# Kernel tuning notes

Hardware: AMD Instinct MI355X
Metric: run time of the kernel (lower is better)

The kernel has to match this reference:

```python
import jax, jax.numpy as jnp
import numpy as np

B, T, D = 8, 1024, 768
H, DH = 12, 64
E, K, DFF = 16, 2, 3072
EPS = 1e-5


def _ln(x, w, b):
    m = x.mean(-1, keepdims=True)
    v = ((x - m) ** 2).mean(-1, keepdims=True)
    return (x - m) * jax.lax.rsqrt(v + EPS) * w + b


def setup_inputs() -> dict:
    key = jax.random.key(0)
    ks = jax.random.split(key, 12)
    s = 0.02
    return {
        "x": jax.random.normal(ks[0], (B, T, D), jnp.float32),
        "ln1_w": jnp.ones((D,), jnp.float32),
        "ln1_b": jnp.zeros((D,), jnp.float32),
        "qkv_w": jax.random.normal(ks[1], (D, 3 * D), jnp.float32) * s,
        "qkv_b": jnp.zeros((3 * D,), jnp.float32),
        "proj_w": jax.random.normal(ks[2], (D, D), jnp.float32) * s,
        "proj_b": jnp.zeros((D,), jnp.float32),
        "ln2_w": jnp.ones((D,), jnp.float32),
        "ln2_b": jnp.zeros((D,), jnp.float32),
        "router_w": jax.random.normal(ks[3], (D, E), jnp.float32) * s,
        "w1": jax.random.normal(ks[4], (E, D, DFF), jnp.float32) * s,
        "b1": jnp.zeros((E, DFF), jnp.float32),
        "w2": jax.random.normal(ks[5], (E, DFF, D), jnp.float32) * s,
        "b2": jnp.zeros((E, D), jnp.float32),
    }


def _block(x, ln1_w, ln1_b, qkv_w, qkv_b, proj_w, proj_b,
           ln2_w, ln2_b, router_w, w1, b1, w2, b2):
    # --- attention ---
    h = _ln(x, ln1_w, ln1_b)
    qkv = h @ qkv_w + qkv_b                      # [B,T,3D]
    q, k, v = jnp.split(qkv, 3, axis=-1)
    q = q.reshape(B, T, H, DH).transpose(0, 2, 1, 3)
    k = k.reshape(B, T, H, DH).transpose(0, 2, 1, 3)
    v = v.reshape(B, T, H, DH).transpose(0, 2, 1, 3)
    scores = jnp.einsum("bhqd,bhkd->bhqk", q, k) / np.sqrt(DH)
    causal = jnp.tril(jnp.ones((T, T), bool))
    scores = jnp.where(causal, scores, -jnp.inf)
    attn = jax.nn.softmax(scores, axis=-1)
    y = jnp.einsum("bhqk,bhkd->bhqd", attn, v)
    y = y.transpose(0, 2, 1, 3).reshape(B, T, D)
    x = x + y @ proj_w + proj_b                  # residual 1

    # --- MoE FFN (dense all-experts, gated combine) ---
    z = _ln(x, ln2_w, ln2_b)                     # [B,T,D]
    probs = jax.nn.softmax(z @ router_w, axis=-1)  # [B,T,E]
    top_p, ix = jax.lax.top_k(probs, K)
    gate = (jax.nn.one_hot(ix, E, dtype=probs.dtype) * top_p[..., None]).sum(-2)  # [B,T,E]
    gate_e = jnp.moveaxis(gate, -1, 0)           # [E,B,T]

    def body(acc, ew):
        g, W1, B1, W2, B2 = ew
        out = jax.nn.gelu(z @ W1 + B1, approximate=False) @ W2 + B2
        return acc + g[..., None] * out, None

    yff, _ = jax.lax.scan(body, jnp.zeros_like(z), (gate_e, w1, b1, w2, b2))
    # MoELayer returns z + yff; Block adds x again (faithful double residual)
    return x + z + yff


def reference(x, ln1_w, ln1_b, qkv_w, qkv_b, proj_w, proj_b,
              ln2_w, ln2_b, router_w, w1, b1, w2, b2):
    return _block(x, ln1_w, ln1_b, qkv_w, qkv_b, proj_w, proj_b,
                  ln2_w, ln2_b, router_w, w1, b1, w2, b2)
```

## Files before the change

### kernel.cpp

```cpp
#include <hip/hip_runtime.h>
#include <math.h>

#define D_MODEL 768
#define T_SEQ   1024
#define B_BATCH 8
#define NTOK    8192
#define H_HEADS 12
#define DHEAD   64
#define NEXP    16
#define DFF     3072
#define NPAIR   16384
#define MAXT128 144
#define MAXT256 80

typedef unsigned short u16;
typedef unsigned int   u32;

typedef __attribute__((ext_vector_type(8))) short bf16x8;
typedef __attribute__((ext_vector_type(4))) float f32x4;
typedef __attribute__((ext_vector_type(4))) u32   u32x4;

__device__ __forceinline__ float bf2f(u16 u) { return __uint_as_float(((u32)u) << 16); }
__device__ __forceinline__ u16 f2bf(float f) {
    u32 u = __float_as_uint(f);
    return (u16)((u + 0x7FFFu + ((u >> 16) & 1u)) >> 16);
}

__device__ __forceinline__ void gload16(const void* g, void* l) {
    __builtin_amdgcn_global_load_lds((const __attribute__((address_space(1))) void*)g,
                                     (__attribute__((address_space(3))) void*)l, 16, 0, 0);
}

__global__ __launch_bounds__(256) void ln_kernel(const float* __restrict__ x,
                                                 const float* __restrict__ w,
                                                 const float* __restrict__ b,
                                                 u16* __restrict__ out_bf,
                                                 float* __restrict__ out_f) {
    const int row = blockIdx.x;
    const int tid = threadIdx.x;
    const float* xr = x + (size_t)row * D_MODEL;
    float v0 = xr[tid], v1 = xr[tid + 256], v2 = xr[tid + 512];
    float s = v0 + v1 + v2;
    float s2 = v0 * v0 + v1 * v1 + v2 * v2;
#pragma unroll
    for (int o = 32; o > 0; o >>= 1) { s += __shfl_down(s, o); s2 += __shfl_down(s2, o); }
    __shared__ float red[8];
    __shared__ float stats[2];
    const int wid = tid >> 6;
    if ((tid & 63) == 0) { red[wid] = s; red[4 + wid] = s2; }
    __syncthreads();
    if (tid == 0) {
        float ts = red[0] + red[1] + red[2] + red[3];
        float ts2 = red[4] + red[5] + red[6] + red[7];
        float mean = ts * (1.0f / D_MODEL);
        float var = ts2 * (1.0f / D_MODEL) - mean * mean;
        stats[0] = mean;
        stats[1] = rsqrtf(var + 1e-5f);
    }
    __syncthreads();
    const float mean = stats[0], rstd = stats[1];
    u16* orow = out_bf + (size_t)row * D_MODEL;
    float r0 = (v0 - mean) * rstd * w[tid]       + b[tid];
    float r1 = (v1 - mean) * rstd * w[tid + 256] + b[tid + 256];
    float r2 = (v2 - mean) * rstd * w[tid + 512] + b[tid + 512];
    orow[tid] = f2bf(r0); orow[tid + 256] = f2bf(r1); orow[tid + 512] = f2bf(r2);
    if (out_f) {
        float* frow = out_f + (size_t)row * D_MODEL;
        frow[tid] = r0; frow[tid + 256] = r1; frow[tid + 512] = r2;
    }
}

__global__ __launch_bounds__(256) void transpose_cvt(const float* __restrict__ src,
                                                     u16* __restrict__ dst,
                                                     int R, int C) {
    const size_t plane = (size_t)R * C;
    src += (size_t)blockIdx.z * plane;
    dst += (size_t)blockIdx.z * plane;
    __shared__ __align__(16) u16 tile[64][72];
    const int t = threadIdx.x;
    const int r0 = blockIdx.y * 64, c0 = blockIdx.x * 64;
    {
        const int lr = t >> 2, lc = (t & 3) * 16;
        const float* sp = src + (size_t)(r0 + lr) * C + c0 + lc;
        u16 tmp[16];
#pragma unroll
        for (int j = 0; j < 4; ++j) {
            f32x4 f = *(const f32x4*)(sp + j * 4);
            tmp[j * 4 + 0] = f2bf(f[0]); tmp[j * 4 + 1] = f2bf(f[1]);
            tmp[j * 4 + 2] = f2bf(f[2]); tmp[j * 4 + 3] = f2bf(f[3]);
        }
        *(u32x4*)&tile[lr][lc]     = *(const u32x4*)&tmp[0];
        *(u32x4*)&tile[lr][lc + 8] = *(const u32x4*)&tmp[8];
    }
    __syncthreads();
    {
        const int ln = t >> 2, lk0 = (t & 3) * 16;
        u16 o[16];
#pragma unroll
        for (int j = 0; j < 16; ++j) o[j] = tile[lk0 + j][ln];
        u16* d = dst + (size_t)(c0 + ln) * R + r0 + lk0;
        *(u32x4*)&d[0] = *(const u32x4*)&o[0];
        *(u32x4*)&d[8] = *(const u32x4*)&o[8];
    }
}

template <int MODE>
__global__ __launch_bounds__(512, 4) void gemm256(
    const u16* __restrict__ A, const u16* __restrict__ Bt,
    const float* __restrict__ bias, void* __restrict__ Cout,
    const float* __restrict__ resid,
    const int* __restrict__ bucket_tok, const int* __restrict__ offsets,
    const int* __restrict__ counts, const int* __restrict__ desc_e,
    const int* __restrict__ desc_r, const int* __restrict__ tile_cnt,
    int K, int N)
{
    int e = 0, r0 = 0, off = 0, ne = 0, row0 = 0;
    const int col0 = blockIdx.x * 128;
    if constexpr (MODE >= 2) {
        if ((int)blockIdx.y >= *tile_cnt) return;
        e = desc_e[blockIdx.y];
        r0 = desc_r[blockIdx.y];
        off = offsets[e];
        ne = counts[e];
    } else {
        row0 = blockIdx.y * 256;
    }
    if constexpr (MODE == 2) Bt += (size_t)e * D_MODEL * DFF;
    if constexpr (MODE == 3) Bt += (size_t)e * DFF * D_MODEL;

    __shared__ __align__(16) u16 As[256 * 64];
    __shared__ __align__(16) u16 Bs[128 * 64];

    const int tid = threadIdx.x;
    const int lane = tid & 63;
    const int w = tid >> 6;
    const int wm = w >> 1, wn = w & 1;
    const int fr = lane & 15, fg = lane >> 4;

    const int koff = ((((tid & 7) * 16) ^ (((tid >> 3) & 7) << 4)) >> 1);

    u32 aoff[4];
#pragma unroll
    for (int i = 0; i < 4; ++i) {
        const int r = i * 64 + (tid >> 3);
        u32 row;
        if constexpr (MODE == 2) {
            int rb = r0 + r;
            row = (u32)bucket_tok[off + (rb < ne ? rb : 0)];
        } else if constexpr (MODE == 3) {
            int rb = r0 + r;
            row = (u32)(off + (rb < ne ? rb : (ne - 1)));
        } else {
            row = (u32)(row0 + r);
        }
        aoff[i] = row * (u32)K + (u32)koff;
    }
    u32 boff[2];
#pragma unroll
    for (int i = 0; i < 2; ++i) {
        const int n = i * 64 + (tid >> 3);
        boff[i] = (u32)(col0 + n) * (u32)K + (u32)koff;
    }

    f32x4 acc[4][4] = {};

    for (int k0 = 0; k0 < K; k0 += 64) {
        __syncthreads();
#pragma unroll
        for (int i = 0; i < 4; ++i)
            gload16(A + aoff[i] + k0, &As[(i * 512 + w * 64) * 8]);
#pragma unroll
        for (int i = 0; i < 2; ++i)
            gload16(Bt + boff[i] + k0, &Bs[(i * 512 + w * 64) * 8]);
        __syncthreads();
#pragma unroll
        for (int kk = 0; kk < 2; ++kk) {
            const int sw = ((kk * 64 + fg * 16) ^ ((fr & 7) << 4)) >> 1;
            bf16x8 a[4], b[4];
#pragma unroll
            for (int mi = 0; mi < 4; ++mi)
                a[mi] = *(const bf16x8*)&As[(wm * 64 + mi * 16 + fr) * 64 + sw];
#pragma unroll
            for (int ni = 0; ni < 4; ++ni)
                b[ni] = *(const bf16x8*)&Bs[(wn * 64 + ni * 16 + fr) * 64 + sw];
#pragma unroll
            for (int mi = 0; mi < 4; ++mi)
#pragma unroll
                for (int ni = 0; ni < 4; ++ni)
                    acc[mi][ni] = __builtin_amdgcn_mfma_f32_16x16x32_bf16(a[mi], b[ni], acc[mi][ni], 0, 0, 0);
        }
    }

#pragma unroll
    for (int mi = 0; mi < 4; ++mi) {
#pragma unroll
        for (int ni = 0; ni < 4; ++ni) {
            const int lr = wm * 64 + mi * 16 + fg * 4;
            const int col = col0 + wn * 64 + ni * 16 + fr;
#pragma unroll
            for (int i = 0; i < 4; ++i) {
                float v = acc[mi][ni][i];
                if constexpr (MODE == 0) {
                    int grow = row0 + lr + i;
                    ((u16*)Cout)[(size_t)grow * N + col] = f2bf(v + bias[col]);
                } else if constexpr (MODE == 1) {
                    int grow = row0 + lr + i;
                    size_t idx = (size_t)grow * N + col;
                    ((float*)Cout)[idx] = resid[idx] + v + bias[col];
                } else if constexpr (MODE == 2) {
                    int rb = r0 + lr + i;
                    if (rb < ne) {
                        float vb = v + bias[(size_t)e * DFF + col];
                        float g = 0.5f * vb * (1.0f + erff(vb * 0.70710678118654752f));
                        ((u16*)Cout)[(size_t)(off + rb) * N + col] = f2bf(g);
                    }
                } else {
                    int rb = r0 + lr + i;
                    if (rb < ne) {
                        ((float*)Cout)[(size_t)(off + rb) * N + col] = v + bias[(size_t)e * D_MODEL + col];
                    }
                }
            }
        }
    }
}

template <int MODE>
__global__ __launch_bounds__(256) void gemm128f(
    const u16* __restrict__ A, const float* __restrict__ Bf,
    const float* __restrict__ bias, void* __restrict__ Cout,
    const float* __restrict__ resid,
    const int* __restrict__ bucket_tok, const int* __restrict__ offsets,
    const int* __restrict__ counts, const int* __restrict__ desc_e,
    const int* __restrict__ desc_r, const int* __restrict__ tile_cnt,
    int K, int N)
{
    int e = 0, r0 = 0, off = 0, ne = 0, row0 = 0;
    const int col0 = blockIdx.x * 128;
    if constexpr (MODE >= 2) {
        if ((int)blockIdx.y >= *tile_cnt) return;
        e = desc_e[blockIdx.y]; r0 = desc_r[blockIdx.y];
        off = offsets[e]; ne = counts[e];
    } else row0 = blockIdx.y * 128;
    if constexpr (MODE == 2) Bf += (size_t)e * D_MODEL * DFF;
    if constexpr (MODE == 3) Bf += (size_t)e * DFF * D_MODEL;

    __shared__ __align__(16) u16 AsL[128 * 32];
    __shared__ __align__(16) u16 BsL[128 * 32];

    const int tid = threadIdx.x;
    const int lane = tid & 63;
    const int w = tid >> 6;
    const int wr = (w >> 1) * 64, wc = (w & 1) * 64;
    const int fr = lane & 15, fg = lane >> 4;
    const int lrow = lane >> 2, lk = (lane & 3) * 8;

    const u16* ag[2];
#pragma unroll
    for (int i = 0; i < 2; ++i) {
        int r = i * 64 + w * 16 + lrow;
        size_t srow;
        if constexpr (MODE == 2) {
            int rb = r0 + r;
            int tok = bucket_tok[off + (rb < ne ? rb : 0)];
            srow = (size_t)tok * K;
        } else if constexpr (MODE == 3) {
            int rb = r0 + r;
            int pp = off + (rb < ne ? rb : (ne - 1));
            srow = (size_t)pp * K;
        } else srow = (size_t)(row0 + r) * K;
        ag[i] = A + srow + lk;
    }

    f32x4 acc[4][4] = {};
    for (int k0 = 0; k0 < K; k0 += 32) {
        __syncthreads();
        gload16(ag[0] + k0, &AsL[0 * 2048 + w * 512]);
        gload16(ag[1] + k0, &AsL[1 * 2048 + w * 512]);
#pragma unroll
        for (int i = 0; i < 4; ++i) {
            int s = tid + 256 * i;
            int kk = s >> 5, n4 = (s & 31) * 4;
            f32x4 f = *(const f32x4*)(Bf + (size_t)(k0 + kk) * N + col0 + n4);
            BsL[(n4 + 0) * 32 + kk] = f2bf(f[0]);
            BsL[(n4 + 1) * 32 + kk] = f2bf(f[1]);
            BsL[(n4 + 2) * 32 + kk] = f2bf(f[2]);
            BsL[(n4 + 3) * 32 + kk] = f2bf(f[3]);
        }
        __syncthreads();
        bf16x8 a[4], b[4];
#pragma unroll
        for (int mi = 0; mi < 4; ++mi)
            a[mi] = *(const bf16x8*)&AsL[(wr + mi * 16 + fr) * 32 + fg * 8];
#pragma unroll
        for (int ni = 0; ni < 4; ++ni)
            b[ni] = *(const bf16x8*)&BsL[(wc + ni * 16 + fr) * 32 + fg * 8];
#pragma unroll
        for (int mi = 0; mi < 4; ++mi)
#pragma unroll
            for (int ni = 0; ni < 4; ++ni)
                acc[mi][ni] = __builtin_amdgcn_mfma_f32_16x16x32_bf16(a[mi], b[ni], acc[mi][ni], 0, 0, 0);
    }
#pragma unroll
    for (int mi = 0; mi < 4; ++mi) {
#pragma unroll
        for (int ni = 0; ni < 4; ++ni) {
            const int lr = wr + mi * 16 + fg * 4;
            const int col = col0 + wc + ni * 16 + fr;
#pragma unroll
            for (int i = 0; i < 4; ++i) {
                float v = acc[mi][ni][i];
                if constexpr (MODE == 0) {
                    int grow = row0 + lr + i;
                    ((u16*)Cout)[(size_t)grow * N + col] = f2bf(v + bias[col]);
                } else if constexpr (MODE == 1) {
                    int grow = row0 + lr + i;
                    size_t idx = (size_t)grow * N + col;
                    ((float*)Cout)[idx] = resid[idx] + v + bias[col];
                } else if constexpr (MODE == 2) {
                    int rb = r0 + lr + i;
                    if (rb < ne) {
                        float vb = v + bias[(size_t)e * DFF + col];
                        float g = 0.5f * vb * (1.0f + erff(vb * 0.70710678118654752f));
                        ((u16*)Cout)[(size_t)(off + rb) * N + col] = f2bf(g);
                    }
                } else {
                    int rb = r0 + lr + i;
                    if (rb < ne) {
                        ((float*)Cout)[(size_t)(off + rb) * N + col] = v + bias[(size_t)e * D_MODEL + col];
                    }
                }
            }
        }
    }
}

__global__ __launch_bounds__(256) void attn_mfma(const u16* __restrict__ qkv,
                                                 u16* __restrict__ y) {
    const int bh = blockIdx.x;
    const int b = bh / H_HEADS, h = bh % H_HEADS;
    const int qt = gridDim.y - 1 - blockIdx.y;
    const int tid = threadIdx.x, lane = tid & 63, w = tid >> 6;
    const int fr = lane & 15, fg = lane >> 4;

    __shared__ __align__(16) u16 Ks[64][72];
    __shared__ __align__(16) u16 Vt[64][72];
    __shared__ __align__(16) u16 Ps[4][16][72];

    const int tb = b * T_SEQ + qt * 64;

    bf16x8 aq[2];
    {
        const u16* qp = qkv + (size_t)(tb + w * 16 + fr) * (3 * D_MODEL) + h * DHEAD + fg * 8;
        aq[0] = *(const bf16x8*)qp;
        aq[1] = *(const bf16x8*)(qp + 32);
    }
    f32x4 accO[4] = {};
    float m_[4], l_[4];
#pragma unroll
    for (int i = 0; i < 4; ++i) { m_[i] = -1e30f; l_[i] = 0.0f; }

    for (int kt = 0; kt <= qt; ++kt) {
        __syncthreads();
        {
            const int krow = tid >> 2, c16 = (tid & 3) * 16;
            const u16* kp = qkv + (size_t)(b * T_SEQ + kt * 64 + krow) * (3 * D_MODEL)
                          + D_MODEL + h * DHEAD + c16;
            *(u32x4*)&Ks[krow][c16]     = *(const u32x4*)kp;
            *(u32x4*)&Ks[krow][c16 + 8] = *(const u32x4*)(kp + 8);
            const u16* vp = kp + D_MODEL;
            u16 vv[16];
            *(u32x4*)&vv[0] = *(const u32x4*)vp;
            *(u32x4*)&vv[8] = *(const u32x4*)(vp + 8);
#pragma unroll
            for (int j = 0; j < 16; ++j) Vt[c16 + j][krow] = vv[j];
        }
        __syncthreads();

        f32x4 s4[4] = {};
#pragma unroll
        for (int kk = 0; kk < 2; ++kk) {
#pragma unroll
            for (int ni = 0; ni < 4; ++ni) {
                bf16x8 bk = *(const bf16x8*)&Ks[ni * 16 + fr][kk * 32 + fg * 8];
                s4[ni] = __builtin_amdgcn_mfma_f32_16x16x32_bf16(aq[kk], bk, s4[ni], 0, 0, 0);
            }
        }

        const bool diag = (kt == qt);
        float p[4][4];
#pragma unroll
        for (int i = 0; i < 4; ++i) {
            const int rloc = w * 16 + fg * 4 + i;
            float rmax = -1e30f;
#pragma unroll
            for (int ni = 0; ni < 4; ++ni) {
                float v = s4[ni][i] * 0.125f;
                if (diag && (ni * 16 + fr) > rloc) v = -1e30f;
                p[ni][i] = v;
                rmax = fmaxf(rmax, v);
            }
#pragma unroll
            for (int msk = 1; msk < 16; msk <<= 1) rmax = fmaxf(rmax, __shfl_xor(rmax, msk));
            const float mn = fmaxf(m_[i], rmax);
            float sum = 0.0f;
#pragma unroll
            for (int ni = 0; ni < 4; ++ni) {
                float ev = __expf(p[ni][i] - mn);
                p[ni][i] = ev;
                sum += ev;
            }
#pragma unroll
            for (int msk = 1; msk < 16; msk <<= 1) sum += __shfl_xor(sum, msk);
            const float sc = __expf(m_[i] - mn);
            l_[i] = l_[i] * sc + sum;
            m_[i] = mn;
#pragma unroll
            for (int ni = 0; ni < 4; ++ni) accO[ni][i] *= sc;
        }

#pragma unroll
        for (int i = 0; i < 4; ++i)
#pragma unroll
            for (int ni = 0; ni < 4; ++ni)
                Ps[w][fg * 4 + i][ni * 16 + fr] = f2bf(p[ni][i]);

#pragma unroll
        for (int kk = 0; kk < 2; ++kk) {
            bf16x8 ap = *(const bf16x8*)&Ps[w][fr][kk * 32 + fg * 8];
#pragma unroll
            for (int ni = 0; ni < 4; ++ni) {
                bf16x8 bv = *(const bf16x8*)&Vt[ni * 16 + fr][kk * 32 + fg * 8];
                accO[ni] = __builtin_amdgcn_mfma_f32_16x16x32_bf16(ap, bv, accO[ni], 0, 0, 0);
            }
        }
    }

#pragma unroll
    for (int i = 0; i < 4; ++i) {
        const float inv = 1.0f / l_[i];
        u16* yp = y + (size_t)(tb + w * 16 + fg * 4 + i) * D_MODEL + h * DHEAD;
#pragma unroll
        for (int ni = 0; ni < 4; ++ni) yp[ni * 16 + fr] = f2bf(accO[ni][i] * inv);
    }
}

__global__ __launch_bounds__(64) void router_kernel(const float* __restrict__ z,
                                                    const float* __restrict__ rw,
                                                    float* __restrict__ gates,
                                                    int* __restrict__ eidx) {
    const int t = blockIdx.x;
    const int lane = threadIdx.x;
    const int e = lane & 15, part = lane >> 4;
    const float* zr = z + (size_t)t * D_MODEL;
    float acc = 0.0f;
    for (int d = part * 192; d < part * 192 + 192; ++d)
        acc += zr[d] * rw[d * NEXP + e];
    acc += __shfl_down(acc, 32);
    acc += __shfl_down(acc, 16);
    const float lg = acc;
    float logit[NEXP];
#pragma unroll
    for (int ee = 0; ee < NEXP; ++ee) logit[ee] = __shfl(lg, ee);
    if (lane == 0) {
        float m1 = -1e30f, m2 = -1e30f; int i1 = 0, i2 = 0;
#pragma unroll
        for (int ee = 0; ee < NEXP; ++ee) {
            float v = logit[ee];
            if (v > m1) { m2 = m1; i2 = i1; m1 = v; i1 = ee; }
            else if (v > m2) { m2 = v; i2 = ee; }
        }
        float den = 0.0f;
#pragma unroll
        for (int ee = 0; ee < NEXP; ++ee) den += __expf(logit[ee] - m1);
        const float inv = 1.0f / den;
        gates[2 * t] = inv;
        gates[2 * t + 1] = __expf(m2 - m1) * inv;
        eidx[2 * t] = i1;
        eidx[2 * t + 1] = i2;
    }
}

__global__ __launch_bounds__(256) void count_kernel(const int* __restrict__ eidx, int* counts) {
    int i = blockIdx.x * 256 + threadIdx.x;
    if (i < NPAIR) atomicAdd(&counts[eidx[i]], 1);
}

__global__ void offsets_kernel(const int* __restrict__ counts, int* offsets, int* cursor,
                               int* desc_e, int* desc_r, int* tile_cnt, int step) {
    if (threadIdx.x == 0 && blockIdx.x == 0) {
        int off = 0, nt = 0;
        for (int e = 0; e < NEXP; ++e) {
            offsets[e] = off;
            cursor[e] = off;
            int c = counts[e];
            for (int r = 0; r < c; r += step) { desc_e[nt] = e; desc_r[nt] = r; ++nt; }
            off += c;
        }
        *tile_cnt = nt;
    }
}

__global__ __launch_bounds__(256) void scatter_kernel(const int* __restrict__ eidx, int* cursor,
                                                      int* __restrict__ btok, int* __restrict__ ppos) {
    int i = blockIdx.x * 256 + threadIdx.x;
    if (i < NPAIR) {
        int pos = atomicAdd(&cursor[eidx[i]], 1);
        btok[pos] = i >> 1;
        ppos[i] = pos;
    }
}

__global__ __launch_bounds__(256) void final_kernel(const float* __restrict__ x1,
                                                    const float* __restrict__ zf,
                                                    const float* __restrict__ moe_o,
                                                    const float* __restrict__ gates,
                                                    const int* __restrict__ ppos,
                                                    float* __restrict__ out) {
    const int t = blockIdx.x;
    const int d = blockIdx.y * 256 + threadIdx.x;
    const size_t idx = (size_t)t * D_MODEL + d;
    const float g0 = gates[2 * t], g1 = gates[2 * t + 1];
    const int p0 = ppos[2 * t], p1 = ppos[2 * t + 1];
    out[idx] = x1[idx] + zf[idx] + g0 * moe_o[(size_t)p0 * D_MODEL + d]
                                 + g1 * moe_o[(size_t)p1 * D_MODEL + d];
}

extern "C" void kernel_launch(void* const* d_in, const int* in_sizes, int n_in,
                              void* d_out, int out_size, void* d_ws, size_t ws_size,
                              hipStream_t stream) {
    const float* x        = (const float*)d_in[0];
    const float* ln1_w    = (const float*)d_in[1];
    const float* ln1_b    = (const float*)d_in[2];
    const float* qkv_w    = (const float*)d_in[3];
    const float* qkv_b    = (const float*)d_in[4];
    const float* proj_w   = (const float*)d_in[5];
    const float* proj_b   = (const float*)d_in[6];
    const float* ln2_w    = (const float*)d_in[7];
    const float* ln2_b    = (const float*)d_in[8];
    const float* router_w = (const float*)d_in[9];
    const float* w1       = (const float*)d_in[10];
    const float* b1       = (const float*)d_in[11];
    const float* w2       = (const float*)d_in[12];
    const float* b2       = (const float*)d_in[13];
    float* out = (float*)d_out;

    char* ws = (char*)d_ws;
    size_t off = 0;
    auto alloc = [&](size_t bytes) -> void* {
        void* p = ws + off;
        off += (bytes + 255) & ~(size_t)255;
        return p;
    };
    u16*  h_bf   = (u16*)alloc((size_t)NTOK * D_MODEL * 2);
    u16*  qkv_bf = (u16*)alloc((size_t)NTOK * 3 * D_MODEL * 2);
    u16*  y_bf   = h_bf;
    float* x1    = (float*)alloc((size_t)NTOK * D_MODEL * 4);
    u16*  z_bf   = (u16*)alloc((size_t)NTOK * D_MODEL * 2);
    float* z_f   = (float*)alloc((size_t)NTOK * D_MODEL * 4);
    u16*  act    = (u16*)alloc((size_t)NPAIR * DFF * 2);
    float* moe_o = (float*)alloc((size_t)NPAIR * D_MODEL * 4);
    float* gates = (float*)alloc((size_t)NTOK * 2 * 4);
    int*  eidx   = (int*)alloc((size_t)NTOK * 2 * 4);
    int*  ppos   = (int*)alloc((size_t)NTOK * 2 * 4);
    int*  btok   = (int*)alloc((size_t)NPAIR * 4);
    int*  counts = (int*)alloc(NEXP * 4);
    int*  offs   = (int*)alloc(NEXP * 4);
    int*  cursor = (int*)alloc(NEXP * 4);
    int*  desc_e = (int*)alloc(MAXT128 * 4);
    int*  desc_r = (int*)alloc(MAXT128 * 4);
    int*  tcnt   = (int*)alloc(4);
    u16* qkvT  = (u16*)alloc((size_t)(3 * D_MODEL) * D_MODEL * 2);
    u16* projT = (u16*)alloc((size_t)D_MODEL * D_MODEL * 2);
    u16* w1t   = (u16*)alloc((size_t)NEXP * DFF * D_MODEL * 2);
    u16* w2t   = (u16*)alloc((size_t)NEXP * D_MODEL * DFF * 2);
    const bool useT = (off <= ws_size);
    (void)in_sizes; (void)n_in; (void)out_size;

    hipMemsetAsync(counts, 0, NEXP * 4, stream);

    if (useT) {
        transpose_cvt<<<dim3(3 * D_MODEL / 64, D_MODEL / 64, 1), 256, 0, stream>>>(qkv_w, qkvT, D_MODEL, 3 * D_MODEL);
        transpose_cvt<<<dim3(D_MODEL / 64, D_MODEL / 64, 1), 256, 0, stream>>>(proj_w, projT, D_MODEL, D_MODEL);
        transpose_cvt<<<dim3(DFF / 64, D_MODEL / 64, NEXP), 256, 0, stream>>>(w1, w1t, D_MODEL, DFF);
        transpose_cvt<<<dim3(D_MODEL / 64, DFF / 64, NEXP), 256, 0, stream>>>(w2, w2t, DFF, D_MODEL);
    }

    ln_kernel<<<NTOK, 256, 0, stream>>>(x, ln1_w, ln1_b, h_bf, nullptr);
    if (useT)
        gemm256<0><<<dim3(18, 32), 512, 0, stream>>>(h_bf, qkvT, qkv_b, qkv_bf, nullptr,
            nullptr, nullptr, nullptr, nullptr, nullptr, nullptr, D_MODEL, 3 * D_MODEL);
    else
        gemm128f<0><<<dim3(18, 64), 256, 0, stream>>>(h_bf, qkv_w, qkv_b, qkv_bf, nullptr,
            nullptr, nullptr, nullptr, nullptr, nullptr, nullptr, D_MODEL, 3 * D_MODEL);

    attn_mfma<<<dim3(B_BATCH * H_HEADS, T_SEQ / 64), 256, 0, stream>>>(qkv_bf, y_bf);

    if (useT)
        gemm256<1><<<dim3(6, 32), 512, 0, stream>>>(y_bf, projT, proj_b, x1, x,
            nullptr, nullptr, nullptr, nullptr, nullptr, nullptr, D_MODEL, D_MODEL);
    else
        gemm128f<1><<<dim3(6, 64), 256, 0, stream>>>(y_bf, proj_w, proj_b, x1, x,
            nullptr, nullptr, nullptr, nullptr, nullptr, nullptr, D_MODEL, D_MODEL);

    ln_kernel<<<NTOK, 256, 0, stream>>>(x1, ln2_w, ln2_b, z_bf, z_f);
    router_kernel<<<NTOK, 64, 0, stream>>>(z_f, router_w, gates, eidx);
    count_kernel<<<NPAIR / 256, 256, 0, stream>>>(eidx, counts);
    offsets_kernel<<<1, 64, 0, stream>>>(counts, offs, cursor, desc_e, desc_r, tcnt,
                                         useT ? 256 : 128);
    scatter_kernel<<<NPAIR / 256, 256, 0, stream>>>(eidx, cursor, btok, ppos);

    if (useT) {
        gemm256<2><<<dim3(DFF / 128, MAXT256), 512, 0, stream>>>(z_bf, w1t, b1, act, nullptr,
            btok, offs, counts, desc_e, desc_r, tcnt, D_MODEL, DFF);
        gemm256<3><<<dim3(D_MODEL / 128, MAXT256), 512, 0, stream>>>(act, w2t, b2, moe_o, nullptr,
            btok, offs, counts, desc_e, desc_r, tcnt, DFF, D_MODEL);
    } else {
        gemm128f<2><<<dim3(DFF / 128, MAXT128), 256, 0, stream>>>(z_bf, w1, b1, act, nullptr,
            btok, offs, counts, desc_e, desc_r, tcnt, D_MODEL, DFF);
        gemm128f<3><<<dim3(D_MODEL / 128, MAXT128), 256, 0, stream>>>(act, w2, b2, moe_o, nullptr,
            btok, offs, counts, desc_e, desc_r, tcnt, DFF, D_MODEL);
    }

    final_kernel<<<dim3(NTOK, 3), 256, 0, stream>>>(x1, z_f, moe_o, gates, ppos, out);
}
```

Before: 699.0 us.

## Double-buffer LDS tiles in gemm256 to overlap global loads with MFMA

```diff
diff --git a/kernel.cpp b/kernel.cpp
--- a/kernel.cpp
+++ b/kernel.cpp
@@ -105,7 +105,7 @@
 }
 
 template <int MODE>
-__global__ __launch_bounds__(512, 4) void gemm256(
+__global__ __launch_bounds__(512, 2) void gemm256(
     const u16* __restrict__ A, const u16* __restrict__ Bt,
     const float* __restrict__ bias, void* __restrict__ Cout,
     const float* __restrict__ resid,
@@ -128,8 +128,8 @@
     if constexpr (MODE == 2) Bt += (size_t)e * D_MODEL * DFF;
     if constexpr (MODE == 3) Bt += (size_t)e * DFF * D_MODEL;
 
-    __shared__ __align__(16) u16 As[256 * 64];
-    __shared__ __align__(16) u16 Bs[128 * 64];
+    __shared__ __align__(16) u16 As[2][256 * 64];
+    __shared__ __align__(16) u16 Bs[2][128 * 64];
 
     const int tid = threadIdx.x;
     const int lane = tid & 63;
@@ -164,31 +164,47 @@
 
     f32x4 acc[4][4] = {};
 
-    for (int k0 = 0; k0 < K; k0 += 64) {
-        __syncthreads();
-#pragma unroll
-        for (int i = 0; i < 4; ++i)
-            gload16(A + aoff[i] + k0, &As[(i * 512 + w * 64) * 8]);
-#pragma unroll
-        for (int i = 0; i < 2; ++i)
-            gload16(Bt + boff[i] + k0, &Bs[(i * 512 + w * 64) * 8]);
-        __syncthreads();
+    const int nt = K >> 6;
+#pragma unroll
+    for (int i = 0; i < 4; ++i)
+        gload16(A + aoff[i], &As[0][(i * 512 + w * 64) * 8]);
+#pragma unroll
+    for (int i = 0; i < 2; ++i)
+        gload16(Bt + boff[i], &Bs[0][(i * 512 + w * 64) * 8]);
+    asm volatile("s_waitcnt vmcnt(0)" ::: "memory");
+    __builtin_amdgcn_s_barrier();
+
+    int cur = 0;
+    for (int t = 0; t < nt; ++t) {
+        if (t + 1 < nt) {
+            const int k0n = (t + 1) * 64;
+            const int nxt = cur ^ 1;
+#pragma unroll
+            for (int i = 0; i < 4; ++i)
+                gload16(A + aoff[i] + k0n, &As[nxt][(i * 512 + w * 64) * 8]);
+#pragma unroll
+            for (int i = 0; i < 2; ++i)
+                gload16(Bt + boff[i] + k0n, &Bs[nxt][(i * 512 + w * 64) * 8]);
+        }
 #pragma unroll
         for (int kk = 0; kk < 2; ++kk) {
             const int sw = ((kk * 64 + fg * 16) ^ ((fr & 7) << 4)) >> 1;
             bf16x8 a[4], b[4];
 #pragma unroll
             for (int mi = 0; mi < 4; ++mi)
-                a[mi] = *(const bf16x8*)&As[(wm * 64 + mi * 16 + fr) * 64 + sw];
+                a[mi] = *(const bf16x8*)&As[cur][(wm * 64 + mi * 16 + fr) * 64 + sw];
 #pragma unroll
             for (int ni = 0; ni < 4; ++ni)
-                b[ni] = *(const bf16x8*)&Bs[(wn * 64 + ni * 16 + fr) * 64 + sw];
+                b[ni] = *(const bf16x8*)&Bs[cur][(wn * 64 + ni * 16 + fr) * 64 + sw];
 #pragma unroll
             for (int mi = 0; mi < 4; ++mi)
 #pragma unroll
                 for (int ni = 0; ni < 4; ++ni)
                     acc[mi][ni] = __builtin_amdgcn_mfma_f32_16x16x32_bf16(a[mi], b[ni], acc[mi][ni], 0, 0, 0);
         }
+        asm volatile("s_waitcnt vmcnt(0)" ::: "memory");
+        __builtin_amdgcn_s_barrier();
+        cur ^= 1;
     }
 
 #pragma unroll
```

After: 818.4 us. 1.17x slower.

## Double-buffer LDS in GEMM and add 256-wide N tiles

Applied to the files above, without the earlier changes.

```diff
diff --git a/kernel.cpp b/kernel.cpp
--- a/kernel.cpp
+++ b/kernel.cpp
@@ -29,6 +29,13 @@
 __device__ __forceinline__ void gload16(const void* g, void* l) {
     __builtin_amdgcn_global_load_lds((const __attribute__((address_space(1))) void*)g,
                                      (__attribute__((address_space(3))) void*)l, 16, 0, 0);
+}
+
+template <int N>
+__device__ __forceinline__ void wait_vm() {
+    if constexpr (N == 0) asm volatile("s_waitcnt vmcnt(0)" ::: "memory");
+    else if constexpr (N == 6) asm volatile("s_waitcnt vmcnt(6)" ::: "memory");
+    else asm volatile("s_waitcnt vmcnt(8)" ::: "memory");
 }
 
 __global__ __launch_bounds__(256) void ln_kernel(const float* __restrict__ x,
@@ -104,8 +111,8 @@
     }
 }
 
-template <int MODE>
-__global__ __launch_bounds__(512, 4) void gemm256(
+template <int MODE, int NB>
+__global__ __launch_bounds__(512, 2) void gemmT(
     const u16* __restrict__ A, const u16* __restrict__ Bt,
     const float* __restrict__ bias, void* __restrict__ Cout,
     const float* __restrict__ resid,
@@ -114,8 +121,14 @@
     const int* __restrict__ desc_r, const int* __restrict__ tile_cnt,
     int K, int N)
 {
+    constexpr int WN = (NB == 256) ? 4 : 2;
+    constexpr int MI = (NB == 256) ? 8 : 4;
+    constexpr int NI = 4;
+    constexpr int BG = NB / 64;
+    constexpr int G  = 4 + BG;
+
     int e = 0, r0 = 0, off = 0, ne = 0, row0 = 0;
-    const int col0 = blockIdx.x * 128;
+    const int col0 = blockIdx.x * NB;
     if constexpr (MODE >= 2) {
         if ((int)blockIdx.y >= *tile_cnt) return;
         e = desc_e[blockIdx.y];
@@ -128,13 +141,13 @@
     if constexpr (MODE == 2) Bt += (size_t)e * D_MODEL * DFF;
     if constexpr (MODE == 3) Bt += (size_t)e * DFF * D_MODEL;
 
-    __shared__ __align__(16) u16 As[256 * 64];
-    __shared__ __align__(16) u16 Bs[128 * 64];
+    __shared__ __align__(16) u16 As[2][256 * 64];
+    __shared__ __align__(16) u16 Bs[2][NB * 64];
 
     const int tid = threadIdx.x;
     const int lane = tid & 63;
     const int w = tid >> 6;
-    const int wm = w >> 1, wn = w & 1;
+    const int wm = w / WN, wn = w % WN;
     const int fr = lane & 15, fg = lane >> 4;
 
     const int koff = ((((tid & 7) * 16) ^ (((tid >> 3) & 7) << 4)) >> 1);
@@ -155,47 +168,66 @@
         }
         aoff[i] = row * (u32)K + (u32)koff;
     }
-    u32 boff[2];
-#pragma unroll
-    for (int i = 0; i < 2; ++i) {
+    u32 boff[BG];
+#pragma unroll
+    for (int i = 0; i < BG; ++i) {
         const int n = i * 64 + (tid >> 3);
         boff[i] = (u32)(col0 + n) * (u32)K + (u32)koff;
     }
 
-    f32x4 acc[4][4] = {};
-
-    for (int k0 = 0; k0 < K; k0 += 64) {
-        __syncthreads();
+    auto stage = [&](int buf, int k0) {
 #pragma unroll
         for (int i = 0; i < 4; ++i)
-            gload16(A + aoff[i] + k0, &As[(i * 512 + w * 64) * 8]);
-#pragma unroll
-        for (int i = 0; i < 2; ++i)
-            gload16(Bt + boff[i] + k0, &Bs[(i * 512 + w * 64) * 8]);
-        __syncthreads();
+            gload16(A + aoff[i] + k0, &As[buf][(i * 512 + w * 64) * 8]);
+#pragma unroll
+        for (int i = 0; i < BG; ++i)
+            gload16(Bt + boff[i] + k0, &Bs[buf][(i * 512 + w * 64) * 8]);
+    };
+
+    f32x4 acc[MI][NI] = {};
+    const int nt = K >> 6;
+
+    stage(0, 0);
+    if (nt > 1) { stage(1, 64); wait_vm<G>(); }
+    else wait_vm<0>();
+    __builtin_amdgcn_s_barrier();
+
+    for (int t = 0; t < nt; ++t) {
+        const u16* Ac = As[t & 1];
+        const u16* Bc = Bs[t & 1];
 #pragma unroll
         for (int kk = 0; kk < 2; ++kk) {
             const int sw = ((kk * 64 + fg * 16) ^ ((fr & 7) << 4)) >> 1;
-            bf16x8 a[4], b[4];
-#pragma unroll
-            for (int mi = 0; mi < 4; ++mi)
-                a[mi] = *(const bf16x8*)&As[(wm * 64 + mi * 16 + fr) * 64 + sw];
-#pragma unroll
-            for (int ni = 0; ni < 4; ++ni)
-                b[ni] = *(const bf16x8*)&Bs[(wn * 64 + ni * 16 + fr) * 64 + sw];
-#pragma unroll
-            for (int mi = 0; mi < 4; ++mi)
-#pragma unroll
-                for (int ni = 0; ni < 4; ++ni)
+            bf16x8 a[MI], b[NI];
+#pragma unroll
+            for (int mi = 0; mi < MI; ++mi)
+                a[mi] = *(const bf16x8*)&Ac[(wm * (MI * 16) + mi * 16 + fr) * 64 + sw];
+#pragma unroll
+            for (int ni = 0; ni < NI; ++ni)
+                b[ni] = *(const bf16x8*)&Bc[(wn * 64 + ni * 16 + fr) * 64 + sw];
+#pragma unroll
+            for (int mi = 0; mi < MI; ++mi)
+#pragma unroll
+                for (int ni = 0; ni < NI; ++ni)
                     acc[mi][ni] = __builtin_amdgcn_mfma_f32_16x16x32_bf16(a[mi], b[ni], acc[mi][ni], 0, 0, 0);
         }
-    }
-
-#pragma unroll
-    for (int mi = 0; mi < 4; ++mi) {
-#pragma unroll
-        for (int ni = 0; ni < 4; ++ni) {
-            const int lr = wm * 64 + mi * 16 + fg * 4;
+        if (t == nt - 1) break;
+        __builtin_amdgcn_s_barrier();
+        asm volatile("" ::: "memory");
+        if (t + 2 < nt) {
+            stage(t & 1, (t + 2) * 64);
+            wait_vm<G>();
+        } else {
+            wait_vm<0>();
+        }
+        __builtin_amdgcn_s_barrier();
+    }
+
+#pragma unroll
+    for (int mi = 0; mi < MI; ++mi) {
+#pragma unroll
+        for (int ni = 0; ni < NI; ++ni) {
+            const int lr = wm * (MI * 16) + mi * 16 + fg * 4;
             const int col = col0 + wn * 64 + ni * 16 + fr;
 #pragma unroll
             for (int i = 0; i < 4; ++i) {
@@ -588,7 +620,7 @@
 
     ln_kernel<<<NTOK, 256, 0, stream>>>(x, ln1_w, ln1_b, h_bf, nullptr);
     if (useT)
-        gemm256<0><<<dim3(18, 32), 512, 0, stream>>>(h_bf, qkvT, qkv_b, qkv_bf, nullptr,
+        gemmT<0, 256><<<dim3(9, 32), 512, 0, stream>>>(h_bf, qkvT, qkv_b, qkv_bf, nullptr,
             nullptr, nullptr, nullptr, nullptr, nullptr, nullptr, D_MODEL, 3 * D_MODEL);
     else
         gemm128f<0><<<dim3(18, 64), 256, 0, stream>>>(h_bf, qkv_w, qkv_b, qkv_bf, nullptr,
@@ -597,7 +629,7 @@
     attn_mfma<<<dim3(B_BATCH * H_HEADS, T_SEQ / 64), 256, 0, stream>>>(qkv_bf, y_bf);
 
     if (useT)
-        gemm256<1><<<dim3(6, 32), 512, 0, stream>>>(y_bf, projT, proj_b, x1, x,
+        gemmT<1, 128><<<dim3(6, 32), 512, 0, stream>>>(y_bf, projT, proj_b, x1, x,
             nullptr, nullptr, nullptr, nullptr, nullptr, nullptr, D_MODEL, D_MODEL);
     else
         gemm128f<1><<<dim3(6, 64), 256, 0, stream>>>(y_bf, proj_w, proj_b, x1, x,
@@ -611,9 +643,9 @@
     scatter_kernel<<<NPAIR / 256, 256, 0, stream>>>(eidx, cursor, btok, ppos);
 
     if (useT) {
-        gemm256<2><<<dim3(DFF / 128, MAXT256), 512, 0, stream>>>(z_bf, w1t, b1, act, nullptr,
+        gemmT<2, 256><<<dim3(DFF / 256, MAXT256), 512, 0, stream>>>(z_bf, w1t, b1, act, nullptr,
             btok, offs, counts, desc_e, desc_r, tcnt, D_MODEL, DFF);
-        gemm256<3><<<dim3(D_MODEL / 128, MAXT256), 512, 0, stream>>>(act, w2t, b2, moe_o, nullptr,
+        gemmT<3, 256><<<dim3(D_MODEL / 256, MAXT256), 512, 0, stream>>>(act, w2t, b2, moe_o, nullptr,
             btok, offs, counts, desc_e, desc_r, tcnt, DFF, D_MODEL);
     } else {
         gemm128f<2><<<dim3(DFF / 128, MAXT128), 256, 0, stream>>>(z_bf, w1, b1, act, nullptr,
```

Result: slower. 786.2 us (+12.5%).
